# Kernel optimization log

Hardware: AMD Instinct MI355X
Metric: run time of the kernel (lower is better)

## Reference

```python
import jax, jax.numpy as jnp
import numpy as np

B, Q, L = 64, 64, 8192
KC = 51            # NarrowConv1D kernel size
HC = KC // 2 + 1   # 26 raw symmetric-half params
N = 500
KT = N + 1         # 501 transpose-conv kernel size
HT = KT // 2 + 1   # 251 raw half params

@jax.custom_vjp
def sigmoid_st(u):
    # Sigmoid forward, straight-through (identity) backward
    return jax.nn.sigmoid(u)

def _sst_fwd(u):
    return jax.nn.sigmoid(u), None

def _sst_bwd(res, g):
    return (g,)

sigmoid_st.defvjp(_sst_fwd, _sst_bwd)

def symmetric(w):
    # cat(X, X[..., :-1].flip(-1)) -> symmetric kernel of odd length
    return jnp.concatenate([w, w[..., :-1][..., ::-1]], axis=-1)

def depthwise_conv(x, k, pad):
    # x: [B, Q, L]; k: [Q, K] one kernel per channel (groups == channels)
    return jax.lax.conv_general_dilated(
        x, k[:, None, :], window_strides=(1,), padding=[(pad, pad)],
        dimension_numbers=("NCH", "OIH", "NCH"), feature_group_count=x.shape[1])

def setup_inputs() -> dict:
    key = jax.random.key(0)
    k1, k2, k3, k4 = jax.random.split(key, 4)
    return {
        "x": jax.random.normal(k1, (B, Q, L), dtype=jnp.float32),
        "conv_w_half": jax.random.normal(k2, (HC,), dtype=jnp.float32) * 0.1,
        "tc_w_half": jax.random.normal(k3, (Q, HT), dtype=jnp.float32),
        "A_raw": jax.random.normal(k4, (Q,), dtype=jnp.float32),
    }

def reference(x, conv_w_half, tc_w_half, A_raw):
    # 1) NarrowConv1D: one symmetric kernel shared across all Q channels
    kc = symmetric(conv_w_half)                       # [51]
    kc_full = jnp.broadcast_to(kc, (Q, KC))           # ChannelSame expand
    x = depthwise_conv(x, kc_full, KC // 2)           # [B,Q,L], 'same'

    # 2) softmax over spectral axis
    x = jax.nn.softmax(x, axis=-1)

    # 3) SymmetricNormConvTranspose1d: sigmoid(straight-through) + symmetric;
    #    stride-1 transpose conv with symmetric kernel == depthwise conv with
    #    padding K-1-p = N//2
    wt = sigmoid_st(tc_w_half)                        # [Q, 251] in (0,1)
    kt = symmetric(wt)                                # [Q, 501]
    x = depthwise_conv(x, kt, N // 2)                 # [B,Q,L]

    # 4) serial lattice (reflection/transmission) recursion over Q channels
    a = sigmoid_st(A_raw)                             # [Q]
    xs = jnp.transpose(x, (1, 0, 2))                  # [Q,B,L]

    def step(carry, inp):
        r, t2 = carry
        rn, aq = inp
        tn = 1.0 - rn
        s = 1.0 / (1.0 - aq * r * rn)
        r_new = r + aq * rn * t2 * s
        t2_new = aq * t2 * tn * tn * s * s
        return (r_new, t2_new), None

    init = (jnp.zeros_like(xs[0]), jnp.ones_like(xs[0]))
    (r, _), _ = jax.lax.scan(step, init, (xs, a))

    peak = wt[-1, -1]                                 # weight[-1,0,N//2] (kernel center)
    r = r / (peak * jnp.prod(a))
    return r                                          # [B, L]
```

## Files before the change

### kernel.cpp

```cpp
#include <hip/hip_runtime.h>

#define B_ 64
#define Q_ 64
#define L_ 8192
#define KCONV 51
#define HC 26
#define HT 251
#define NCH2 34
#define NCH1 6
#define TAL_CH 28

#define A51_OFF 512
#define TA_OFF  8192
#define RN_OFF  2236416

#define MAPB(s) ((((s) & ~7) | ((((s) & 7) + ((s) >> 3)) & 7)) << 4)

typedef _Float16 f16x8 __attribute__((ext_vector_type(8)));
typedef float f32x16 __attribute__((ext_vector_type(16)));
typedef const __attribute__((address_space(1))) void cg_void;
typedef __attribute__((address_space(3))) void lds_void3;

__device__ __forceinline__ float sigm(float v) {
    return 1.0f / (1.0f + __expf(-v));
}

__global__ __launch_bounds__(256) void k_params(const float* __restrict__ cwh,
                                                const float* __restrict__ tcw,
                                                const float* __restrict__ araw,
                                                float* __restrict__ ws) {
    const int tid = threadIdx.x;
    const int q = blockIdx.x;
    char* wsb = (char*)ws;
    if (q < Q_) {
        for (int idx = tid; idx < NCH2 * 64; idx += 256) {
            int c = idx >> 6, lane = idx & 63;
            int hi = lane >> 5, i = lane & 31;
            int mbase = 16 * c + 8 * hi - i - 6;
            f16x8 hv;
            #pragma unroll
            for (int jj = 0; jj < 8; jj++) {
                int m = mbase + jj;
                float v = 0.0f;
                if (m >= 0 && m <= 500) {
                    int hh = (m <= 250) ? m : (500 - m);
                    v = sigm(tcw[q * HT + hh]);
                }
                hv[jj] = (_Float16)v;
            }
            *(f16x8*)(wsb + TA_OFF + ((size_t)q * (NCH2 * 64) + idx) * 16) = hv;
        }
    } else {
        if (tid < Q_) ws[tid] = sigm(araw[tid]);
        for (int idx = tid; idx < NCH1 * 64; idx += 256) {
            int c = idx >> 6, lane = idx & 63;
            int hi = lane >> 5, i = lane & 31;
            int mbase = 16 * c + 8 * hi - i - 7;
            f16x8 hv;
            #pragma unroll
            for (int jj = 0; jj < 8; jj++) {
                int m = mbase + jj;
                float v = 0.0f;
                if (m >= 0 && m < KCONV) v = cwh[m < HC ? m : (KCONV - 1 - m)];
                hv[jj] = (_Float16)v;
            }
            *(f16x8*)(wsb + A51_OFF + idx * 16) = hv;
        }
        __syncthreads();
        if (tid == 0) {
            float p = 1.0f;
            for (int j = 0; j < Q_; j++) p *= ws[j];
            float peak = sigm(tcw[(Q_ - 1) * HT + 250]);
            ws[64] = 1.0f / (peak * p);
        }
    }
}

__global__ __launch_bounds__(512, 4) void k_fused(const float* __restrict__ x,
                                                  float* __restrict__ ws) {
    const int tid = threadIdx.x;
    const int bid = blockIdx.x;
    const int q = bid >> 5, pr = bid & 31;
    const int row0 = (2 * pr) * Q_ + q, row1 = (2 * pr + 1) * Q_ + q;
    char* wsb = (char*)ws;
    __shared__ __attribute__((aligned(128))) char bufA[17408];
    __shared__ __attribute__((aligned(128))) char bufB[17408];
    __shared__ __attribute__((aligned(128))) char TAL[TAL_CH * 1024];
    __shared__ float red[32];

    const int w = tid >> 6, lane = tid & 63, j = lane & 31, hi = lane >> 5;

    {
        const char* tabg = wsb + TA_OFF + (size_t)q * (NCH2 * 64) * 16;
        for (int c = w; c < TAL_CH; c += 8) {
            const void* gp = tabg + (c * 64 + lane) * 16;
            __builtin_amdgcn_global_load_lds((cg_void*)gp,
                                             (lds_void3*)(TAL + c * 1024), 16, 0, 0);
        }
    }

    f16x8 a51r[NCH1];
    #pragma unroll
    for (int c = 0; c < NCH1; c++)
        a51r[c] = *(const f16x8*)(wsb + A51_OFF + (c * 64 + lane) * 16);

    const uint4 z4 = {0u, 0u, 0u, 0u};
    if (tid < 32) {
        *(uint4*)(bufA + MAPB(tid)) = z4;
        *(uint4*)(bufB + MAPB(tid)) = z4;
    } else if (tid >= 64 && tid < 96) {
        int s = 1056 + (tid - 64);
        *(uint4*)(bufA + MAPB(s)) = z4;
        *(uint4*)(bufB + MAPB(s)) = z4;
    }

    union H8 { _Float16 h[8]; uint4 u; };
    {
        #pragma unroll
        for (int r = 0; r < 2; r++) {
            const float* xr = x + (size_t)(r ? row1 : row0) * L_ + 16 * tid;
            char* buf = r ? bufB : bufA;
            float4 f0 = *(const float4*)(xr + 0);
            float4 f1 = *(const float4*)(xr + 4);
            float4 f2 = *(const float4*)(xr + 8);
            float4 f3 = *(const float4*)(xr + 12);
            H8 h0, h1;
            h0.h[0] = (_Float16)f0.x; h0.h[1] = (_Float16)f0.y;
            h0.h[2] = (_Float16)f0.z; h0.h[3] = (_Float16)f0.w;
            h0.h[4] = (_Float16)f1.x; h0.h[5] = (_Float16)f1.y;
            h0.h[6] = (_Float16)f1.z; h0.h[7] = (_Float16)f1.w;
            h1.h[0] = (_Float16)f2.x; h1.h[1] = (_Float16)f2.y;
            h1.h[2] = (_Float16)f2.z; h1.h[3] = (_Float16)f2.w;
            h1.h[4] = (_Float16)f3.x; h1.h[5] = (_Float16)f3.y;
            h1.h[6] = (_Float16)f3.z; h1.h[7] = (_Float16)f3.w;
            *(uint4*)(buf + MAPB(2 * tid + 32)) = h0.u;
            *(uint4*)(buf + MAPB(2 * tid + 33)) = h1.u;
        }
    }
    __syncthreads();

    f32x16 acc0 = {}, acc1 = {};
    {
        f16x8 pA[2], pB[2];
        pA[0] = *(const f16x8*)(bufA + MAPB(128 * w + 4 * j + 28 + hi));
        pB[0] = *(const f16x8*)(bufB + MAPB(128 * w + 4 * j + 28 + hi));
        pA[1] = *(const f16x8*)(bufA + MAPB(128 * w + 4 * j + 30 + hi));
        pB[1] = *(const f16x8*)(bufB + MAPB(128 * w + 4 * j + 30 + hi));
        #pragma unroll
        for (int c = 0; c < NCH1; c++) {
            acc0 = __builtin_amdgcn_mfma_f32_32x32x16_f16(a51r[c], pA[c & 1], acc0, 0, 0, 0);
            acc1 = __builtin_amdgcn_mfma_f32_32x32x16_f16(a51r[c], pB[c & 1], acc1, 0, 0, 0);
            if (c + 2 < NCH1) {
                const int bo = MAPB(128 * w + 4 * j + 2 * (c + 2) + 28 + hi);
                pA[c & 1] = *(const f16x8*)(bufA + bo);
                pB[c & 1] = *(const f16x8*)(bufB + bo);
            }
        }
    }

    float mx0 = -3.402823466e+38f, mx1 = -3.402823466e+38f;
    #pragma unroll
    for (int e = 0; e < 16; e++) { mx0 = fmaxf(mx0, acc0[e]); mx1 = fmaxf(mx1, acc1[e]); }
    #pragma unroll
    for (int o = 32; o > 0; o >>= 1) {
        mx0 = fmaxf(mx0, __shfl_xor(mx0, o));
        mx1 = fmaxf(mx1, __shfl_xor(mx1, o));
    }
    float sm0 = 0.0f, sm1 = 0.0f;
    #pragma unroll
    for (int e = 0; e < 16; e++) {
        acc0[e] = __expf(acc0[e] - mx0); sm0 += acc0[e];
        acc1[e] = __expf(acc1[e] - mx1); sm1 += acc1[e];
    }
    #pragma unroll
    for (int o = 32; o > 0; o >>= 1) { sm0 += __shfl_xor(sm0, o); sm1 += __shfl_xor(sm1, o); }
    if (lane == 0) {
        red[w] = mx0; red[8 + w] = sm0;
        red[16 + w] = mx1; red[24 + w] = sm1;
    }
    __syncthreads();
    float mg0 = red[0], mg1 = red[16];
    #pragma unroll
    for (int i = 1; i < 8; i++) { mg0 = fmaxf(mg0, red[i]); mg1 = fmaxf(mg1, red[16 + i]); }
    float ss0 = 0.0f, ss1 = 0.0f;
    #pragma unroll
    for (int i = 0; i < 8; i++) {
        ss0 += red[8 + i] * __expf(red[i] - mg0);
        ss1 += red[24 + i] * __expf(red[16 + i] - mg1);
    }
    const float isum0 = __expf(mx0 - mg0) / ss0;
    const float isum1 = __expf(mx1 - mg1) / ss1;

    union P4 { _Float16 h[4]; uint2 u; };
    #pragma unroll
    for (int k = 0; k < 4; k++) {
        P4 p0, p1;
        #pragma unroll
        for (int d = 0; d < 4; d++) {
            p0.h[d] = (_Float16)(acc0[4 * k + d] * isum0);
            p1.h[d] = (_Float16)(acc1[4 * k + d] * isum1);
        }
        const int bo = MAPB(128 * w + 4 * j + k + 32) + 8 * hi;
        *(uint2*)(bufA + bo) = p0.u;
        *(uint2*)(bufB + bo) = p1.u;
    }
    __syncthreads();

    const char* tab6 = wsb + TA_OFF + ((size_t)q * (NCH2 * 64) + lane) * 16;
    f32x16 o0 = {}, o1 = {};
    {
        f16x8 afr[4], pA[2], pB[2];
        #pragma unroll
        for (int c = 0; c < 4; c++)
            afr[c] = *(const f16x8*)(TAL + c * 1024 + lane * 16);
        #pragma unroll
        for (int c = 0; c < 2; c++) {
            const int bo = MAPB(128 * w + 4 * j + 2 * c + hi);
            pA[c] = *(const f16x8*)(bufA + bo);
            pB[c] = *(const f16x8*)(bufB + bo);
        }
        #pragma unroll
        for (int c = 0; c < NCH2; c++) {
            o0 = __builtin_amdgcn_mfma_f32_32x32x16_f16(afr[c & 3], pA[c & 1], o0, 0, 0, 0);
            o1 = __builtin_amdgcn_mfma_f32_32x32x16_f16(afr[c & 3], pB[c & 1], o1, 0, 0, 0);
            if (c + 2 < NCH2) {
                const int bo = MAPB(128 * w + 4 * j + 2 * (c + 2) + hi);
                pA[c & 1] = *(const f16x8*)(bufA + bo);
                pB[c & 1] = *(const f16x8*)(bufB + bo);
            }
            if (c + 4 < NCH2) {
                afr[c & 3] = (c + 4 < TAL_CH)
                    ? *(const f16x8*)(TAL + (c + 4) * 1024 + lane * 16)
                    : *(const f16x8*)(tab6 + (c + 4) * 1024);
            }
        }
    }
    __syncthreads();

    #pragma unroll
    for (int k = 0; k < 4; k++) {
        P4 p0, p1;
        #pragma unroll
        for (int d = 0; d < 4; d++) {
            p0.h[d] = (_Float16)o0[4 * k + d];
            p1.h[d] = (_Float16)o1[4 * k + d];
        }
        const int bo = MAPB(128 * w + 4 * j + k) + 8 * hi;
        *(uint2*)(bufA + bo) = p0.u;
        *(uint2*)(bufB + bo) = p1.u;
    }
    __syncthreads();
    {
        uint4 r0 = *(uint4*)(bufA + MAPB(2 * tid));
        uint4 r1 = *(uint4*)(bufA + MAPB(2 * tid + 1));
        char* dst = wsb + RN_OFF + ((size_t)row0 * L_ + 16 * tid) * 2;
        *(uint4*)dst = r0;
        *(uint4*)(dst + 16) = r1;
        uint4 r2 = *(uint4*)(bufB + MAPB(2 * tid));
        uint4 r3 = *(uint4*)(bufB + MAPB(2 * tid + 1));
        char* dst1 = wsb + RN_OFF + ((size_t)row1 * L_ + 16 * tid) * 2;
        *(uint4*)dst1 = r2;
        *(uint4*)(dst1 + 16) = r3;
    }
}

__global__ __launch_bounds__(256) void k_lat(const float* __restrict__ ws,
                                             float* __restrict__ out) {
    const int tid = threadIdx.x;
    const int T = blockIdx.x & 7, b = blockIdx.x >> 3;
    const char* wsb = (const char*)ws;
    const int l = 1024 * T + 4 * tid;
    const char* src = wsb + RN_OFF + ((size_t)(b * Q_) * L_ + l) * 2;
    float r[4] = {0.0f, 0.0f, 0.0f, 0.0f};
    float t2[4] = {1.0f, 1.0f, 1.0f, 1.0f};
    union P4 { _Float16 h[4]; uint2 u; };
    P4 cur;
    cur.u = *(const uint2*)src;
    for (int q = 0; q < Q_; q++) {
        P4 nxt = cur;
        if (q < Q_ - 1) nxt.u = *(const uint2*)(src + (size_t)(q + 1) * L_ * 2);
        const float aq = ws[q];
        #pragma unroll
        for (int e = 0; e < 4; e++) {
            float rn = (float)cur.h[e], tn = 1.0f - rn;
            float si = 1.0f / (1.0f - aq * r[e] * rn);
            float rnew = r[e] + aq * rn * t2[e] * si;
            t2[e] = aq * t2[e] * tn * tn * si * si;
            r[e] = rnew;
        }
        cur = nxt;
    }
    const float inv_scale = ws[64];
    float4 o;
    o.x = r[0] * inv_scale; o.y = r[1] * inv_scale;
    o.z = r[2] * inv_scale; o.w = r[3] * inv_scale;
    *(float4*)&out[(size_t)b * L_ + l] = o;
}

extern "C" void kernel_launch(void* const* d_in, const int* in_sizes, int n_in,
                              void* d_out, int out_size, void* d_ws, size_t ws_size,
                              hipStream_t stream) {
    (void)in_sizes; (void)n_in; (void)out_size; (void)ws_size;
    const float* x    = (const float*)d_in[0];
    const float* cwh  = (const float*)d_in[1];
    const float* tcw  = (const float*)d_in[2];
    const float* araw = (const float*)d_in[3];
    float* out = (float*)d_out;
    float* ws  = (float*)d_ws;

    hipLaunchKernelGGL(k_params, dim3(Q_ + 1), dim3(256), 0, stream, cwh, tcw, araw, ws);
    hipLaunchKernelGGL(k_fused, dim3((B_ / 2) * Q_), dim3(512), 0, stream, x, ws);
    hipLaunchKernelGGL(k_lat, dim3(B_ * 8), dim3(256), 0, stream, ws, out);
}
```

Before: 95.37 us.

## Make fused conv blocks persistent over four row pairs and drop LDS filter staging

```diff
diff --git a/kernel.cpp b/kernel.cpp
--- a/kernel.cpp
+++ b/kernel.cpp
@@ -8,7 +8,6 @@
 #define HT 251
 #define NCH2 34
 #define NCH1 6
-#define TAL_CH 28
 
 #define A51_OFF 512
 #define TA_OFF  8192
@@ -18,8 +17,6 @@
 
 typedef _Float16 f16x8 __attribute__((ext_vector_type(8)));
 typedef float f32x16 __attribute__((ext_vector_type(16)));
-typedef const __attribute__((address_space(1))) void cg_void;
-typedef __attribute__((address_space(3))) void lds_void3;
 
 __device__ __forceinline__ float sigm(float v) {
     return 1.0f / (1.0f + __expf(-v));
@@ -79,43 +76,38 @@
 __global__ __launch_bounds__(512, 4) void k_fused(const float* __restrict__ x,
                                                   float* __restrict__ ws) {
     const int tid = threadIdx.x;
-    const int bid = blockIdx.x;
-    const int q = bid >> 5, pr = bid & 31;
-    const int row0 = (2 * pr) * Q_ + q, row1 = (2 * pr + 1) * Q_ + q;
+    const int q = blockIdx.x >> 3, g = blockIdx.x & 7;
     char* wsb = (char*)ws;
     __shared__ __attribute__((aligned(128))) char bufA[17408];
     __shared__ __attribute__((aligned(128))) char bufB[17408];
-    __shared__ __attribute__((aligned(128))) char TAL[TAL_CH * 1024];
     __shared__ float red[32];
 
     const int w = tid >> 6, lane = tid & 63, j = lane & 31, hi = lane >> 5;
-
-    {
-        const char* tabg = wsb + TA_OFF + (size_t)q * (NCH2 * 64) * 16;
-        for (int c = w; c < TAL_CH; c += 8) {
-            const void* gp = tabg + (c * 64 + lane) * 16;
-            __builtin_amdgcn_global_load_lds((cg_void*)gp,
-                                             (lds_void3*)(TAL + c * 1024), 16, 0, 0);
-        }
-    }
-
-    f16x8 a51r[NCH1];
-    #pragma unroll
-    for (int c = 0; c < NCH1; c++)
-        a51r[c] = *(const f16x8*)(wsb + A51_OFF + (c * 64 + lane) * 16);
-
+    const char* tab6 = wsb + TA_OFF + ((size_t)q * (NCH2 * 64) + lane) * 16;
     const uint4 z4 = {0u, 0u, 0u, 0u};
-    if (tid < 32) {
-        *(uint4*)(bufA + MAPB(tid)) = z4;
-        *(uint4*)(bufB + MAPB(tid)) = z4;
-    } else if (tid >= 64 && tid < 96) {
-        int s = 1056 + (tid - 64);
-        *(uint4*)(bufA + MAPB(s)) = z4;
-        *(uint4*)(bufB + MAPB(s)) = z4;
-    }
-
     union H8 { _Float16 h[8]; uint4 u; };
-    {
+    union P4 { _Float16 h[4]; uint2 u; };
+
+    for (int jb = 0; jb < 4; jb++) {
+        const int pr = 4 * g + jb;
+        const int row0 = (2 * pr) * Q_ + q, row1 = (2 * pr + 1) * Q_ + q;
+
+        if (jb) __syncthreads();
+
+        f16x8 a51r[NCH1];
+        #pragma unroll
+        for (int c = 0; c < NCH1; c++)
+            a51r[c] = *(const f16x8*)(wsb + A51_OFF + (c * 64 + lane) * 16);
+
+        if (tid < 32) {
+            *(uint4*)(bufA + MAPB(tid)) = z4;
+            *(uint4*)(bufB + MAPB(tid)) = z4;
+        } else if (tid >= 64 && tid < 96) {
+            int s = 1056 + (tid - 64);
+            *(uint4*)(bufA + MAPB(s)) = z4;
+            *(uint4*)(bufB + MAPB(s)) = z4;
+        }
+
         #pragma unroll
         for (int r = 0; r < 2; r++) {
             const float* xr = x + (size_t)(r ? row1 : row0) * L_ + 16 * tid;
@@ -136,131 +128,126 @@
             *(uint4*)(buf + MAPB(2 * tid + 32)) = h0.u;
             *(uint4*)(buf + MAPB(2 * tid + 33)) = h1.u;
         }
-    }
-    __syncthreads();
-
-    f32x16 acc0 = {}, acc1 = {};
-    {
-        f16x8 pA[2], pB[2];
-        pA[0] = *(const f16x8*)(bufA + MAPB(128 * w + 4 * j + 28 + hi));
-        pB[0] = *(const f16x8*)(bufB + MAPB(128 * w + 4 * j + 28 + hi));
-        pA[1] = *(const f16x8*)(bufA + MAPB(128 * w + 4 * j + 30 + hi));
-        pB[1] = *(const f16x8*)(bufB + MAPB(128 * w + 4 * j + 30 + hi));
-        #pragma unroll
-        for (int c = 0; c < NCH1; c++) {
-            acc0 = __builtin_amdgcn_mfma_f32_32x32x16_f16(a51r[c], pA[c & 1], acc0, 0, 0, 0);
-            acc1 = __builtin_amdgcn_mfma_f32_32x32x16_f16(a51r[c], pB[c & 1], acc1, 0, 0, 0);
-            if (c + 2 < NCH1) {
-                const int bo = MAPB(128 * w + 4 * j + 2 * (c + 2) + 28 + hi);
-                pA[c & 1] = *(const f16x8*)(bufA + bo);
-                pB[c & 1] = *(const f16x8*)(bufB + bo);
-            }
-        }
-    }
-
-    float mx0 = -3.402823466e+38f, mx1 = -3.402823466e+38f;
-    #pragma unroll
-    for (int e = 0; e < 16; e++) { mx0 = fmaxf(mx0, acc0[e]); mx1 = fmaxf(mx1, acc1[e]); }
-    #pragma unroll
-    for (int o = 32; o > 0; o >>= 1) {
-        mx0 = fmaxf(mx0, __shfl_xor(mx0, o));
-        mx1 = fmaxf(mx1, __shfl_xor(mx1, o));
-    }
-    float sm0 = 0.0f, sm1 = 0.0f;
-    #pragma unroll
-    for (int e = 0; e < 16; e++) {
-        acc0[e] = __expf(acc0[e] - mx0); sm0 += acc0[e];
-        acc1[e] = __expf(acc1[e] - mx1); sm1 += acc1[e];
-    }
-    #pragma unroll
-    for (int o = 32; o > 0; o >>= 1) { sm0 += __shfl_xor(sm0, o); sm1 += __shfl_xor(sm1, o); }
-    if (lane == 0) {
-        red[w] = mx0; red[8 + w] = sm0;
-        red[16 + w] = mx1; red[24 + w] = sm1;
-    }
-    __syncthreads();
-    float mg0 = red[0], mg1 = red[16];
-    #pragma unroll
-    for (int i = 1; i < 8; i++) { mg0 = fmaxf(mg0, red[i]); mg1 = fmaxf(mg1, red[16 + i]); }
-    float ss0 = 0.0f, ss1 = 0.0f;
-    #pragma unroll
-    for (int i = 0; i < 8; i++) {
-        ss0 += red[8 + i] * __expf(red[i] - mg0);
-        ss1 += red[24 + i] * __expf(red[16 + i] - mg1);
-    }
-    const float isum0 = __expf(mx0 - mg0) / ss0;
-    const float isum1 = __expf(mx1 - mg1) / ss1;
-
-    union P4 { _Float16 h[4]; uint2 u; };
-    #pragma unroll
-    for (int k = 0; k < 4; k++) {
-        P4 p0, p1;
-        #pragma unroll
-        for (int d = 0; d < 4; d++) {
-            p0.h[d] = (_Float16)(acc0[4 * k + d] * isum0);
-            p1.h[d] = (_Float16)(acc1[4 * k + d] * isum1);
-        }
-        const int bo = MAPB(128 * w + 4 * j + k + 32) + 8 * hi;
-        *(uint2*)(bufA + bo) = p0.u;
-        *(uint2*)(bufB + bo) = p1.u;
-    }
-    __syncthreads();
-
-    const char* tab6 = wsb + TA_OFF + ((size_t)q * (NCH2 * 64) + lane) * 16;
-    f32x16 o0 = {}, o1 = {};
-    {
-        f16x8 afr[4], pA[2], pB[2];
-        #pragma unroll
-        for (int c = 0; c < 4; c++)
-            afr[c] = *(const f16x8*)(TAL + c * 1024 + lane * 16);
-        #pragma unroll
-        for (int c = 0; c < 2; c++) {
-            const int bo = MAPB(128 * w + 4 * j + 2 * c + hi);
-            pA[c] = *(const f16x8*)(bufA + bo);
-            pB[c] = *(const f16x8*)(bufB + bo);
-        }
-        #pragma unroll
-        for (int c = 0; c < NCH2; c++) {
-            o0 = __builtin_amdgcn_mfma_f32_32x32x16_f16(afr[c & 3], pA[c & 1], o0, 0, 0, 0);
-            o1 = __builtin_amdgcn_mfma_f32_32x32x16_f16(afr[c & 3], pB[c & 1], o1, 0, 0, 0);
-            if (c + 2 < NCH2) {
-                const int bo = MAPB(128 * w + 4 * j + 2 * (c + 2) + hi);
-                pA[c & 1] = *(const f16x8*)(bufA + bo);
-                pB[c & 1] = *(const f16x8*)(bufB + bo);
-            }
-            if (c + 4 < NCH2) {
-                afr[c & 3] = (c + 4 < TAL_CH)
-                    ? *(const f16x8*)(TAL + (c + 4) * 1024 + lane * 16)
-                    : *(const f16x8*)(tab6 + (c + 4) * 1024);
-            }
-        }
-    }
-    __syncthreads();
-
-    #pragma unroll
-    for (int k = 0; k < 4; k++) {
-        P4 p0, p1;
-        #pragma unroll
-        for (int d = 0; d < 4; d++) {
-            p0.h[d] = (_Float16)o0[4 * k + d];
-            p1.h[d] = (_Float16)o1[4 * k + d];
-        }
-        const int bo = MAPB(128 * w + 4 * j + k) + 8 * hi;
-        *(uint2*)(bufA + bo) = p0.u;
-        *(uint2*)(bufB + bo) = p1.u;
-    }
-    __syncthreads();
-    {
-        uint4 r0 = *(uint4*)(bufA + MAPB(2 * tid));
-        uint4 r1 = *(uint4*)(bufA + MAPB(2 * tid + 1));
-        char* dst = wsb + RN_OFF + ((size_t)row0 * L_ + 16 * tid) * 2;
-        *(uint4*)dst = r0;
-        *(uint4*)(dst + 16) = r1;
-        uint4 r2 = *(uint4*)(bufB + MAPB(2 * tid));
-        uint4 r3 = *(uint4*)(bufB + MAPB(2 * tid + 1));
-        char* dst1 = wsb + RN_OFF + ((size_t)row1 * L_ + 16 * tid) * 2;
-        *(uint4*)dst1 = r2;
-        *(uint4*)(dst1 + 16) = r3;
+        __syncthreads();
+
+        f32x16 acc0 = {}, acc1 = {};
+        {
+            f16x8 pA[2], pB[2];
+            pA[0] = *(const f16x8*)(bufA + MAPB(128 * w + 4 * j + 28 + hi));
+            pB[0] = *(const f16x8*)(bufB + MAPB(128 * w + 4 * j + 28 + hi));
+            pA[1] = *(const f16x8*)(bufA + MAPB(128 * w + 4 * j + 30 + hi));
+            pB[1] = *(const f16x8*)(bufB + MAPB(128 * w + 4 * j + 30 + hi));
+            #pragma unroll
+            for (int c = 0; c < NCH1; c++) {
+                acc0 = __builtin_amdgcn_mfma_f32_32x32x16_f16(a51r[c], pA[c & 1], acc0, 0, 0, 0);
+                acc1 = __builtin_amdgcn_mfma_f32_32x32x16_f16(a51r[c], pB[c & 1], acc1, 0, 0, 0);
+                if (c + 2 < NCH1) {
+                    const int bo = MAPB(128 * w + 4 * j + 2 * (c + 2) + 28 + hi);
+                    pA[c & 1] = *(const f16x8*)(bufA + bo);
+                    pB[c & 1] = *(const f16x8*)(bufB + bo);
+                }
+            }
+        }
+
+        float mx0 = -3.402823466e+38f, mx1 = -3.402823466e+38f;
+        #pragma unroll
+        for (int e = 0; e < 16; e++) { mx0 = fmaxf(mx0, acc0[e]); mx1 = fmaxf(mx1, acc1[e]); }
+        #pragma unroll
+        for (int o = 32; o > 0; o >>= 1) {
+            mx0 = fmaxf(mx0, __shfl_xor(mx0, o));
+            mx1 = fmaxf(mx1, __shfl_xor(mx1, o));
+        }
+        float sm0 = 0.0f, sm1 = 0.0f;
+        #pragma unroll
+        for (int e = 0; e < 16; e++) {
+            acc0[e] = __expf(acc0[e] - mx0); sm0 += acc0[e];
+            acc1[e] = __expf(acc1[e] - mx1); sm1 += acc1[e];
+        }
+        #pragma unroll
+        for (int o = 32; o > 0; o >>= 1) { sm0 += __shfl_xor(sm0, o); sm1 += __shfl_xor(sm1, o); }
+        if (lane == 0) {
+            red[w] = mx0; red[8 + w] = sm0;
+            red[16 + w] = mx1; red[24 + w] = sm1;
+        }
+        __syncthreads();
+        float mg0 = red[0], mg1 = red[16];
+        #pragma unroll
+        for (int i = 1; i < 8; i++) { mg0 = fmaxf(mg0, red[i]); mg1 = fmaxf(mg1, red[16 + i]); }
+        float ss0 = 0.0f, ss1 = 0.0f;
+        #pragma unroll
+        for (int i = 0; i < 8; i++) {
+            ss0 += red[8 + i] * __expf(red[i] - mg0);
+            ss1 += red[24 + i] * __expf(red[16 + i] - mg1);
+        }
+        const float isum0 = __expf(mx0 - mg0) / ss0;
+        const float isum1 = __expf(mx1 - mg1) / ss1;
+
+        #pragma unroll
+        for (int k = 0; k < 4; k++) {
+            P4 p0, p1;
+            #pragma unroll
+            for (int d = 0; d < 4; d++) {
+                p0.h[d] = (_Float16)(acc0[4 * k + d] * isum0);
+                p1.h[d] = (_Float16)(acc1[4 * k + d] * isum1);
+            }
+            const int bo = MAPB(128 * w + 4 * j + k + 32) + 8 * hi;
+            *(uint2*)(bufA + bo) = p0.u;
+            *(uint2*)(bufB + bo) = p1.u;
+        }
+        __syncthreads();
+
+        f32x16 o0 = {}, o1 = {};
+        {
+            f16x8 afr[4], pA[2], pB[2];
+            #pragma unroll
+            for (int c = 0; c < 4; c++)
+                afr[c] = *(const f16x8*)(tab6 + c * 1024);
+            #pragma unroll
+            for (int c = 0; c < 2; c++) {
+                const int bo = MAPB(128 * w + 4 * j + 2 * c + hi);
+                pA[c] = *(const f16x8*)(bufA + bo);
+                pB[c] = *(const f16x8*)(bufB + bo);
+            }
+            #pragma unroll
+            for (int c = 0; c < NCH2; c++) {
+                o0 = __builtin_amdgcn_mfma_f32_32x32x16_f16(afr[c & 3], pA[c & 1], o0, 0, 0, 0);
+                o1 = __builtin_amdgcn_mfma_f32_32x32x16_f16(afr[c & 3], pB[c & 1], o1, 0, 0, 0);
+                if (c + 2 < NCH2) {
+                    const int bo = MAPB(128 * w + 4 * j + 2 * (c + 2) + hi);
+                    pA[c & 1] = *(const f16x8*)(bufA + bo);
+                    pB[c & 1] = *(const f16x8*)(bufB + bo);
+                }
+                if (c + 4 < NCH2)
+                    afr[c & 3] = *(const f16x8*)(tab6 + (c + 4) * 1024);
+            }
+        }
+        __syncthreads();
+
+        #pragma unroll
+        for (int k = 0; k < 4; k++) {
+            P4 p0, p1;
+            #pragma unroll
+            for (int d = 0; d < 4; d++) {
+                p0.h[d] = (_Float16)o0[4 * k + d];
+                p1.h[d] = (_Float16)o1[4 * k + d];
+            }
+            const int bo = MAPB(128 * w + 4 * j + k) + 8 * hi;
+            *(uint2*)(bufA + bo) = p0.u;
+            *(uint2*)(bufB + bo) = p1.u;
+        }
+        __syncthreads();
+        {
+            uint4 r0 = *(uint4*)(bufA + MAPB(2 * tid));
+            uint4 r1 = *(uint4*)(bufA + MAPB(2 * tid + 1));
+            char* dst = wsb + RN_OFF + ((size_t)row0 * L_ + 16 * tid) * 2;
+            *(uint4*)dst = r0;
+            *(uint4*)(dst + 16) = r1;
+            uint4 r2 = *(uint4*)(bufB + MAPB(2 * tid));
+            uint4 r3 = *(uint4*)(bufB + MAPB(2 * tid + 1));
+            char* dst1 = wsb + RN_OFF + ((size_t)row1 * L_ + 16 * tid) * 2;
+            *(uint4*)dst1 = r2;
+            *(uint4*)(dst1 + 16) = r3;
+        }
     }
 }
 
@@ -309,6 +296,6 @@
     float* ws  = (float*)d_ws;
 
     hipLaunchKernelGGL(k_params, dim3(Q_ + 1), dim3(256), 0, stream, cwh, tcw, araw, ws);
-    hipLaunchKernelGGL(k_fused, dim3((B_ / 2) * Q_), dim3(512), 0, stream, x, ws);
+    hipLaunchKernelGGL(k_fused, dim3(8 * Q_), dim3(512), 0, stream, x, ws);
     hipLaunchKernelGGL(k_lat, dim3(B_ * 8), dim3(256), 0, stream, ws, out);
 }
```

Result: slower. 183.6 us (+92.5%).
